# Kernel optimization log

Hardware: AMD Instinct MI355X
Metric: run time of the kernel (lower is better)

## Reference

```python
import jax, jax.numpy as jnp
import numpy as np

D = 256  # in_channels == out_channels -> output_proj is Identity


def setup_inputs() -> dict:
    key = jax.random.key(0)
    ks = jax.random.split(key, 7)
    B, N = 4, 4096
    s = 1.0 / np.sqrt(D)
    return {
        "x": jax.random.normal(ks[0], (B, N, D), dtype=jnp.float32),
        "Wk": jax.random.normal(ks[1], (D, D), dtype=jnp.float32) * s,
        "bk": jax.random.normal(ks[2], (D,), dtype=jnp.float32) * 0.01,
        "Wq": jax.random.normal(ks[3], (D, D), dtype=jnp.float32) * s,
        "bq": jax.random.normal(ks[4], (D,), dtype=jnp.float32) * 0.01,
        "Wv": jax.random.normal(ks[5], (D, D), dtype=jnp.float32) * s,
        "bv": jax.random.normal(ks[6], (D,), dtype=jnp.float32) * 0.01,
    }


def reference(x, Wk, bk, Wq, bq, Wv, bv):
    # Linear projections: torch Linear(x) = x @ W.T + b; here W is stored as [in, out]
    keys = jnp.einsum("bnd,de->bne", x, Wk) + bk
    queries = jnp.einsum("bnd,de->bne", x, Wq) + bq
    values = jnp.einsum("bnd,de->bne", x, Wv) + bv
    scale = 1.0 / jnp.sqrt(jnp.float32(D))
    scores = jnp.einsum("bqd,bkd->bqk", queries, keys) * scale  # [B, N, N]
    attn = jax.nn.softmax(scores, axis=-1)
    out = jnp.einsum("bqk,bkd->bqd", attn, values)
    return out
```

## Files before the change

kernel.cpp:

```cpp
#include <hip/hip_runtime.h>
#include <hip/hip_bf16.h>


typedef __attribute__((ext_vector_type(8))) short bf16x8;
typedef __attribute__((ext_vector_type(4))) float f32x4;

__device__ __forceinline__ float b2f(ushort u){
  union { uint i; float f; } v; v.i = ((uint)u) << 16; return v.f;
}
__device__ __forceinline__ ushort f2b(float f){
  union { float f; uint i; } v; v.f = f;
  uint i = v.i;
  return (ushort)((i + 0x7FFFu + ((i >> 16) & 1u)) >> 16);
}
__device__ __forceinline__ uint pack2(float a, float b){
  return (uint)f2b(a) | ((uint)f2b(b) << 16);
}
__device__ __forceinline__ uint fbits(float f){
  union { float f; uint i; } v; v.f = f; return v.i;
}

__device__ __forceinline__ void gl_lds16(const ushort* g, ushort* l){
  __builtin_amdgcn_global_load_lds(
      (const __attribute__((address_space(1))) uint*)g,
      (__attribute__((address_space(3))) uint*)l, 16, 0, 0);
}

#define Q_SCALE 0.0901684400555602f
#define FIXED_M 16.0f

__global__ __launch_bounds__(256) void transpose_w_kernel(
    const float* __restrict__ Wk, const float* __restrict__ Wq,
    const float* __restrict__ Wv, ushort* __restrict__ Wt){
  __shared__ ushort t[64][72];
  const float* src = (blockIdx.y == 0) ? Wk : (blockIdx.y == 1) ? Wq : Wv;
  ushort* dst = Wt + blockIdx.y * 65536;
  int tile = blockIdx.x;
  int tr = tile >> 2, tc = tile & 3;
  int tid = threadIdx.x;
  for (int i = tid; i < 1024; i += 256){
    int r = i >> 4, ch = i & 15;
    float4 f = *(const float4*)(src + (tr*64 + r)*256 + tc*64 + ch*4);
    uint2 u; u.x = pack2(f.x, f.y); u.y = pack2(f.z, f.w);
    *(uint2*)&t[r][ch*4] = u;
  }
  __syncthreads();
  for (int i = tid; i < 2048; i += 256){
    int c = i >> 5, r2 = (i & 31)*2;
    uint v = (uint)t[r2][c] | ((uint)t[r2+1][c] << 16);
    *(uint*)(dst + (tc*64 + c)*256 + tr*64 + r2) = v;
  }
}

__global__ __launch_bounds__(256) void proj_kernel(
    const float* __restrict__ x, const ushort* __restrict__ Wt,
    const float* __restrict__ bK, const float* __restrict__ bQ,
    const float* __restrict__ bV,
    ushort* __restrict__ Ko, ushort* __restrict__ Qo, ushort* __restrict__ Vt){
  __shared__ ushort xs[64][264];
  __shared__ ushort wt[2][16][264];
  int my = blockIdx.y;
  int n0 = blockIdx.x * 64;
  const ushort* wsrc = Wt + my*65536;
  const float* bias  = (my==0) ? bK : (my==1) ? bQ : bV;

  int tid = threadIdx.x;
  int lane = tid & 63, w = tid >> 6, quad = lane >> 4, l16 = lane & 15;

  for (int i = tid; i < 4096; i += 256){
    int r = i >> 6, ch = i & 63;
    float4 f = *(const float4*)(x + (size_t)(n0 + r)*256 + ch*4);
    uint2 u; u.x = pack2(f.x, f.y); u.y = pack2(f.z, f.w);
    *(uint2*)&xs[r][ch*4] = u;
  }

  int seg0 = tid*2,     r0 = seg0 >> 5, c0 = seg0 & 31;
  int seg1 = tid*2 + 1, r1 = seg1 >> 5, c1 = seg1 & 31;
  {
    uint4 a = *(const uint4*)(wsrc + r0*256 + c0*8);
    uint4 b = *(const uint4*)(wsrc + r1*256 + c1*8);
    *(uint4*)&wt[0][r0][c0*8] = a;
    *(uint4*)&wt[0][r1][c1*8] = b;
  }
  __syncthreads();

  bf16x8 afr[8];
  #pragma unroll
  for (int ks = 0; ks < 8; ks++)
    afr[ks] = *(const bf16x8*)&xs[w*16 + l16][ks*32 + quad*8];

  for (int nt = 0; nt < 16; nt++){
    int cu = nt & 1;
    uint4 wa, wb;
    if (nt < 15){
      const ushort* wn = wsrc + (nt+1)*4096;
      wa = *(const uint4*)(wn + r0*256 + c0*8);
      wb = *(const uint4*)(wn + r1*256 + c1*8);
    }
    f32x4 acc = {0.f, 0.f, 0.f, 0.f};
    #pragma unroll
    for (int ks = 0; ks < 8; ks++){
      bf16x8 bfr = *(const bf16x8*)&wt[cu][l16][ks*32 + quad*8];
      acc = __builtin_amdgcn_mfma_f32_16x16x32_bf16(afr[ks], bfr, acc, 0, 0, 0);
    }
    int e = nt*16 + l16;
    float bv = bias[e];
    if (my == 2){
      int b  = n0 >> 12;
      int nl = (n0 & 4095) + w*16 + quad*4;
      ushort* vb = Vt + (size_t)b*1048576 + (size_t)e*4096 + nl;
      #pragma unroll
      for (int r = 0; r < 4; r++) vb[r] = f2b(acc[r] + bv);
    } else {
      float scale = (my==1) ? Q_SCALE : 1.0f;
      ushort* out = (my==0) ? Ko : Qo;
      #pragma unroll
      for (int r = 0; r < 4; r++){
        int row = n0 + w*16 + quad*4 + r;
        out[(size_t)row*256 + e] = f2b((acc[r] + bv) * scale);
      }
    }
    if (nt < 15){
      *(uint4*)&wt[cu^1][r0][c0*8] = wa;
      *(uint4*)&wt[cu^1][r1][c1*8] = wb;
    }
    __syncthreads();
  }
}

__global__ __launch_bounds__(256, 2) void attn_kernel(
    const ushort* __restrict__ Q, const ushort* __restrict__ K,
    const ushort* __restrict__ Vt,
    float* __restrict__ O0, ushort* __restrict__ Obf, float* __restrict__ lp){
  __shared__ ushort Kbuf[2][8192];
  __shared__ ushort Vbuf[2][8192];
  __shared__ ushort Ps[128][40];

  int bx   = blockIdx.x;
  int bh   = bx & 15;
  int b    = bh >> 2;
  int half = bh & 3;
  int qt   = bx >> 4;
  int tid = threadIdx.x, lane = tid & 63, w = tid >> 6;
  int quad = lane >> 4, l16 = lane & 15;

  const ushort* Qb = Q  + (size_t)(b*4096 + qt*128)*256;
  const ushort* Kb = K  + (size_t)b*4096*256;
  const ushort* Vb = Vt + (size_t)b*256*4096;

  int kOff[4], vOff[4];
  #pragma unroll
  for (int i = 0; i < 4; i++){
    int off16 = (w*4 + i)*64 + lane;
    int krow = off16 >> 5, ks_ = off16 & 31;
    int g    = ks_ ^ (krow & 7);
    kOff[i]  = krow*256 + g*8;
    int sr = off16 >> 3, sl = off16 & 7;
    int xv = sl ^ (sr & 7);
    int d  = sr*2 + ((xv >> 2) & 1), c = xv & 3;
    vOff[i] = d*4096 + c*8;
  }
  int m7 = l16 & 7;
  int kslot[8];
  #pragma unroll
  for (int ks = 0; ks < 8; ks++) kslot[ks] = ((ks*4 + quad) ^ m7) * 8;
  int vlane = (((l16 >> 1)*8) + (((l16 & 1)*4 + quad) ^ (l16 >> 1))) * 8;

  bf16x8 qf[2][8];
  #pragma unroll
  for (int s = 0; s < 2; s++)
    #pragma unroll
    for (int ks = 0; ks < 8; ks++)
      qf[s][ks] = *(const bf16x8*)(Qb + (size_t)(w*32 + s*16 + l16)*256 + ks*32 + quad*8);

  f32x4 of[2][16];
  #pragma unroll
  for (int s = 0; s < 2; s++)
    #pragma unroll
    for (int dt = 0; dt < 16; dt++) of[s][dt] = (f32x4){0.f, 0.f, 0.f, 0.f};
  float l_i[2][4];
  #pragma unroll
  for (int s = 0; s < 2; s++)
    #pragma unroll
    for (int r = 0; r < 4; r++) l_i[s][r] = 0.f;

  int kt0 = half * 32, kt1 = kt0 + 32;

  #pragma unroll
  for (int i = 0; i < 4; i++){
    gl_lds16(Kb + (size_t)kt0*8192 + kOff[i], &Kbuf[0][(w*4 + i)*512]);
    gl_lds16(Vb + (size_t)kt0*32   + vOff[i], &Vbuf[0][(w*4 + i)*512]);
  }
  __syncthreads();

  int cur = 0;
  for (int kt = kt0; kt < kt1; kt++){
    int nxt = cur ^ 1;
    if (kt + 1 < kt1){
      #pragma unroll
      for (int i = 0; i < 4; i++){
        gl_lds16(Kb + (size_t)(kt+1)*8192 + kOff[i], &Kbuf[nxt][(w*4 + i)*512]);
        gl_lds16(Vb + (size_t)(kt+1)*32   + vOff[i], &Vbuf[nxt][(w*4 + i)*512]);
      }
    }
    const ushort* Kc = &Kbuf[cur][0];
    const ushort* Vc = &Vbuf[cur][0];

    f32x4 sf[2][2];
    #pragma unroll
    for (int s = 0; s < 2; s++)
      #pragma unroll
      for (int nt = 0; nt < 2; nt++) sf[s][nt] = (f32x4){0.f, 0.f, 0.f, 0.f};
    #pragma unroll
    for (int nt = 0; nt < 2; nt++){
      const ushort* Kr = Kc + nt*4096 + l16*256;
      #pragma unroll
      for (int ks = 0; ks < 8; ks++){
        bf16x8 bfr = *(const bf16x8*)(Kr + kslot[ks]);
        sf[0][nt] = __builtin_amdgcn_mfma_f32_16x16x32_bf16(qf[0][ks], bfr, sf[0][nt], 0,0,0);
        sf[1][nt] = __builtin_amdgcn_mfma_f32_16x16x32_bf16(qf[1][ks], bfr, sf[1][nt], 0,0,0);
      }
    }

    #pragma unroll
    for (int s = 0; s < 2; s++){
      #pragma unroll
      for (int r = 0; r < 4; r++){
        float p0 = exp2f(sf[s][0][r] - FIXED_M);
        float p1 = exp2f(sf[s][1][r] - FIXED_M);
        l_i[s][r] += p0 + p1;
        uint pb = __builtin_amdgcn_perm(fbits(p1) + 0x8000u,
                                        fbits(p0) + 0x8000u, 0x07060302u);
        ushort* prow = &Ps[w*32 + s*16 + quad*4 + r][0];
        prow[l16]      = (ushort)pb;
        prow[16 + l16] = (ushort)(pb >> 16);
      }
    }

    bf16x8 pf0 = *(const bf16x8*)&Ps[w*32 +      l16][quad*8];
    bf16x8 pf1 = *(const bf16x8*)&Ps[w*32 + 16 + l16][quad*8];
    #pragma unroll
    for (int dt = 0; dt < 16; dt++){
      bf16x8 vf = *(const bf16x8*)(Vc + dt*512 + vlane);
      of[0][dt] = __builtin_amdgcn_mfma_f32_16x16x32_bf16(pf0, vf, of[0][dt], 0, 0, 0);
      of[1][dt] = __builtin_amdgcn_mfma_f32_16x16x32_bf16(pf1, vf, of[1][dt], 0, 0, 0);
    }

    __syncthreads();
    cur = nxt;
  }

  #pragma unroll
  for (int s = 0; s < 2; s++)
    #pragma unroll
    for (int r = 0; r < 4; r++){
      float rs = l_i[s][r];
      #pragma unroll
      for (int msk = 1; msk < 16; msk <<= 1) rs += __shfl_xor(rs, msk, 16);
      l_i[s][r] = rs;
    }

  #pragma unroll
  for (int s = 0; s < 2; s++){
    int gq0 = b*4096 + qt*128 + w*32 + s*16 + quad*4;
    if (l16 == 0){
      #pragma unroll
      for (int r = 0; r < 4; r++)
        lp[(size_t)half*16384 + gq0 + r] = l_i[s][r];
    }
    if (half == 0){
      #pragma unroll
      for (int dt = 0; dt < 16; dt++)
        #pragma unroll
        for (int r = 0; r < 4; r++)
          O0[(size_t)(gq0 + r)*256 + dt*16 + l16] = of[s][dt][r];
    } else {
      ushort* Oh = Obf + (size_t)(half - 1)*16384*256;
      #pragma unroll
      for (int dt = 0; dt < 16; dt++)
        #pragma unroll
        for (int r = 0; r < 4; r++)
          Oh[(size_t)(gq0 + r)*256 + dt*16 + l16] = f2b(of[s][dt][r]);
    }
  }
}

__global__ __launch_bounds__(256) void merge_kernel(
    float* __restrict__ O0, const ushort* __restrict__ Obf,
    const float* __restrict__ lp){
  int t   = blockIdx.x*256 + threadIdx.x;
  int row = t >> 6;
  int c   = (t & 63) * 4;
  float den = lp[row] + lp[16384 + row] + lp[2*16384 + row] + lp[3*16384 + row];
  float rden = 1.0f / den;
  size_t idx = (size_t)row*256 + c;
  float4 acc = *(float4*)&O0[idx];
  #pragma unroll
  for (int h = 1; h < 4; h++){
    ushort4 oh = *(const ushort4*)&Obf[(size_t)(h-1)*16384*256 + idx];
    acc.x += b2f(oh.x); acc.y += b2f(oh.y);
    acc.z += b2f(oh.z); acc.w += b2f(oh.w);
  }
  acc.x *= rden; acc.y *= rden; acc.z *= rden; acc.w *= rden;
  *(float4*)&O0[idx] = acc;
}

extern "C" void kernel_launch(void* const* d_in, const int* in_sizes, int n_in,
                              void* d_out, int out_size, void* d_ws, size_t ws_size,
                              hipStream_t stream){
  const float* x  = (const float*)d_in[0];
  const float* Wk = (const float*)d_in[1];
  const float* bk = (const float*)d_in[2];
  const float* Wq = (const float*)d_in[3];
  const float* bq = (const float*)d_in[4];
  const float* Wv = (const float*)d_in[5];
  const float* bv = (const float*)d_in[6];

  char* ws = (char*)d_ws;
  ushort* Wt  = (ushort*)(ws);
  ushort* Qb  = (ushort*)(ws + (size_t)1*(1u<<20));
  ushort* Kb  = (ushort*)(ws + (size_t)10*(1u<<20));
  ushort* Vtb = (ushort*)(ws + (size_t)19*(1u<<20));
  ushort* Obf = (ushort*)(ws + (size_t)28*(1u<<20));
  float*  lp  = (float*)(ws + (size_t)54*(1u<<20));

  hipLaunchKernelGGL(transpose_w_kernel, dim3(16, 3), dim3(256), 0, stream,
                     Wk, Wq, Wv, Wt);
  hipLaunchKernelGGL(proj_kernel, dim3(256, 3), dim3(256), 0, stream,
                     x, Wt, bk, bq, bv, Kb, Qb, Vtb);
  hipLaunchKernelGGL(attn_kernel, dim3(512), dim3(256), 0, stream,
                     Qb, Kb, Vtb, (float*)d_out, Obf, lp);
  hipLaunchKernelGGL(merge_kernel, dim3(4096), dim3(256), 0, stream,
                     (float*)d_out, Obf, lp);
}
```

Measured before the change: 203.5 us.

## Split attention work across eight waves per block with one 16-row Q slice each

The attention kernel moves from 256 to 512 threads per block. Each wave now owns a single 16-row query slice instead of two, which halves per-wave accumulator and Q-fragment registers and raises the number of resident waves to hide latency. It also wraps the MFMA phases in s_setprio raises. The cost is that each K/V fragment read from LDS now feeds only one MFMA instead of two, so LDS read traffic per FLOP doubles, and more waves take part in each barrier.

After: 285.1 us. 40.1% more time.

```diff
diff --git a/kernel.cpp b/kernel.cpp
--- a/kernel.cpp
+++ b/kernel.cpp
@@ -128,7 +128,7 @@
   }
 }
 
-__global__ __launch_bounds__(256, 2) void attn_kernel(
+__global__ __launch_bounds__(512, 4) void attn_kernel(
     const ushort* __restrict__ Q, const ushort* __restrict__ K,
     const ushort* __restrict__ Vt,
     float* __restrict__ O0, ushort* __restrict__ Obf, float* __restrict__ lp){
@@ -148,10 +148,10 @@
   const ushort* Kb = K  + (size_t)b*4096*256;
   const ushort* Vb = Vt + (size_t)b*256*4096;
 
-  int kOff[4], vOff[4];
-  #pragma unroll
-  for (int i = 0; i < 4; i++){
-    int off16 = (w*4 + i)*64 + lane;
+  int kOff[2], vOff[2];
+  #pragma unroll
+  for (int i = 0; i < 2; i++){
+    int off16 = (w*2 + i)*64 + lane;
     int krow = off16 >> 5, ks_ = off16 & 31;
     int g    = ks_ ^ (krow & 7);
     kOff[i]  = krow*256 + g*8;
@@ -161,35 +161,26 @@
     vOff[i] = d*4096 + c*8;
   }
   int m7 = l16 & 7;
-  int kslot[8];
-  #pragma unroll
-  for (int ks = 0; ks < 8; ks++) kslot[ks] = ((ks*4 + quad) ^ m7) * 8;
   int vlane = (((l16 >> 1)*8) + (((l16 & 1)*4 + quad) ^ (l16 >> 1))) * 8;
 
-  bf16x8 qf[2][8];
-  #pragma unroll
-  for (int s = 0; s < 2; s++)
-    #pragma unroll
-    for (int ks = 0; ks < 8; ks++)
-      qf[s][ks] = *(const bf16x8*)(Qb + (size_t)(w*32 + s*16 + l16)*256 + ks*32 + quad*8);
-
-  f32x4 of[2][16];
-  #pragma unroll
-  for (int s = 0; s < 2; s++)
-    #pragma unroll
-    for (int dt = 0; dt < 16; dt++) of[s][dt] = (f32x4){0.f, 0.f, 0.f, 0.f};
-  float l_i[2][4];
-  #pragma unroll
-  for (int s = 0; s < 2; s++)
-    #pragma unroll
-    for (int r = 0; r < 4; r++) l_i[s][r] = 0.f;
+  bf16x8 qf[8];
+  #pragma unroll
+  for (int ks = 0; ks < 8; ks++)
+    qf[ks] = *(const bf16x8*)(Qb + (size_t)(w*16 + l16)*256 + ks*32 + quad*8);
+
+  f32x4 of[16];
+  #pragma unroll
+  for (int dt = 0; dt < 16; dt++) of[dt] = (f32x4){0.f, 0.f, 0.f, 0.f};
+  float l_i[4];
+  #pragma unroll
+  for (int r = 0; r < 4; r++) l_i[r] = 0.f;
 
   int kt0 = half * 32, kt1 = kt0 + 32;
 
   #pragma unroll
-  for (int i = 0; i < 4; i++){
-    gl_lds16(Kb + (size_t)kt0*8192 + kOff[i], &Kbuf[0][(w*4 + i)*512]);
-    gl_lds16(Vb + (size_t)kt0*32   + vOff[i], &Vbuf[0][(w*4 + i)*512]);
+  for (int i = 0; i < 2; i++){
+    gl_lds16(Kb + (size_t)kt0*8192 + kOff[i], &Kbuf[0][(w*2 + i)*512]);
+    gl_lds16(Vb + (size_t)kt0*32   + vOff[i], &Vbuf[0][(w*2 + i)*512]);
   }
   __syncthreads();
 
@@ -198,89 +189,82 @@
     int nxt = cur ^ 1;
     if (kt + 1 < kt1){
       #pragma unroll
-      for (int i = 0; i < 4; i++){
-        gl_lds16(Kb + (size_t)(kt+1)*8192 + kOff[i], &Kbuf[nxt][(w*4 + i)*512]);
-        gl_lds16(Vb + (size_t)(kt+1)*32   + vOff[i], &Vbuf[nxt][(w*4 + i)*512]);
+      for (int i = 0; i < 2; i++){
+        gl_lds16(Kb + (size_t)(kt+1)*8192 + kOff[i], &Kbuf[nxt][(w*2 + i)*512]);
+        gl_lds16(Vb + (size_t)(kt+1)*32   + vOff[i], &Vbuf[nxt][(w*2 + i)*512]);
       }
     }
     const ushort* Kc = &Kbuf[cur][0];
     const ushort* Vc = &Vbuf[cur][0];
 
-    f32x4 sf[2][2];
-    #pragma unroll
-    for (int s = 0; s < 2; s++)
-      #pragma unroll
-      for (int nt = 0; nt < 2; nt++) sf[s][nt] = (f32x4){0.f, 0.f, 0.f, 0.f};
+    f32x4 sf[2];
+    sf[0] = (f32x4){0.f, 0.f, 0.f, 0.f};
+    sf[1] = (f32x4){0.f, 0.f, 0.f, 0.f};
+    __builtin_amdgcn_s_setprio(1);
     #pragma unroll
     for (int nt = 0; nt < 2; nt++){
       const ushort* Kr = Kc + nt*4096 + l16*256;
       #pragma unroll
       for (int ks = 0; ks < 8; ks++){
-        bf16x8 bfr = *(const bf16x8*)(Kr + kslot[ks]);
-        sf[0][nt] = __builtin_amdgcn_mfma_f32_16x16x32_bf16(qf[0][ks], bfr, sf[0][nt], 0,0,0);
-        sf[1][nt] = __builtin_amdgcn_mfma_f32_16x16x32_bf16(qf[1][ks], bfr, sf[1][nt], 0,0,0);
+        bf16x8 bfr = *(const bf16x8*)(Kr + (((ks*4 + quad) ^ m7) << 3));
+        sf[nt] = __builtin_amdgcn_mfma_f32_16x16x32_bf16(qf[ks], bfr, sf[nt], 0,0,0);
       }
     }
-
-    #pragma unroll
-    for (int s = 0; s < 2; s++){
-      #pragma unroll
-      for (int r = 0; r < 4; r++){
-        float p0 = exp2f(sf[s][0][r] - FIXED_M);
-        float p1 = exp2f(sf[s][1][r] - FIXED_M);
-        l_i[s][r] += p0 + p1;
-        uint pb = __builtin_amdgcn_perm(fbits(p1) + 0x8000u,
-                                        fbits(p0) + 0x8000u, 0x07060302u);
-        ushort* prow = &Ps[w*32 + s*16 + quad*4 + r][0];
-        prow[l16]      = (ushort)pb;
-        prow[16 + l16] = (ushort)(pb >> 16);
-      }
-    }
-
-    bf16x8 pf0 = *(const bf16x8*)&Ps[w*32 +      l16][quad*8];
-    bf16x8 pf1 = *(const bf16x8*)&Ps[w*32 + 16 + l16][quad*8];
+    __builtin_amdgcn_s_setprio(0);
+
+    #pragma unroll
+    for (int r = 0; r < 4; r++){
+      float p0 = exp2f(sf[0][r] - FIXED_M);
+      float p1 = exp2f(sf[1][r] - FIXED_M);
+      l_i[r] += p0 + p1;
+      uint pb = __builtin_amdgcn_perm(fbits(p1) + 0x8000u,
+                                      fbits(p0) + 0x8000u, 0x07060302u);
+      ushort* prow = &Ps[w*16 + quad*4 + r][0];
+      prow[l16]      = (ushort)pb;
+      prow[16 + l16] = (ushort)(pb >> 16);
+    }
+
+    bf16x8 pf = *(const bf16x8*)&Ps[w*16 + l16][quad*8];
+    __builtin_amdgcn_s_setprio(1);
     #pragma unroll
     for (int dt = 0; dt < 16; dt++){
       bf16x8 vf = *(const bf16x8*)(Vc + dt*512 + vlane);
-      of[0][dt] = __builtin_amdgcn_mfma_f32_16x16x32_bf16(pf0, vf, of[0][dt], 0, 0, 0);
-      of[1][dt] = __builtin_amdgcn_mfma_f32_16x16x32_bf16(pf1, vf, of[1][dt], 0, 0, 0);
-    }
+      of[dt] = __builtin_amdgcn_mfma_f32_16x16x32_bf16(pf, vf, of[dt], 0, 0, 0);
+    }
+    __builtin_amdgcn_s_setprio(0);
 
     __syncthreads();
     cur = nxt;
   }
 
   #pragma unroll
-  for (int s = 0; s < 2; s++)
-    #pragma unroll
-    for (int r = 0; r < 4; r++){
-      float rs = l_i[s][r];
-      #pragma unroll
-      for (int msk = 1; msk < 16; msk <<= 1) rs += __shfl_xor(rs, msk, 16);
-      l_i[s][r] = rs;
-    }
-
-  #pragma unroll
-  for (int s = 0; s < 2; s++){
-    int gq0 = b*4096 + qt*128 + w*32 + s*16 + quad*4;
+  for (int r = 0; r < 4; r++){
+    float rs = l_i[r];
+    #pragma unroll
+    for (int msk = 1; msk < 16; msk <<= 1) rs += __shfl_xor(rs, msk, 16);
+    l_i[r] = rs;
+  }
+
+  {
+    int gq0 = b*4096 + qt*128 + w*16 + quad*4;
     if (l16 == 0){
       #pragma unroll
       for (int r = 0; r < 4; r++)
-        lp[(size_t)half*16384 + gq0 + r] = l_i[s][r];
+        lp[(size_t)half*16384 + gq0 + r] = l_i[r];
     }
     if (half == 0){
       #pragma unroll
       for (int dt = 0; dt < 16; dt++)
         #pragma unroll
         for (int r = 0; r < 4; r++)
-          O0[(size_t)(gq0 + r)*256 + dt*16 + l16] = of[s][dt][r];
+          O0[(size_t)(gq0 + r)*256 + dt*16 + l16] = of[dt][r];
     } else {
       ushort* Oh = Obf + (size_t)(half - 1)*16384*256;
       #pragma unroll
       for (int dt = 0; dt < 16; dt++)
         #pragma unroll
         for (int r = 0; r < 4; r++)
-          Oh[(size_t)(gq0 + r)*256 + dt*16 + l16] = f2b(of[s][dt][r]);
+          Oh[(size_t)(gq0 + r)*256 + dt*16 + l16] = f2b(of[dt][r]);
     }
   }
 }
@@ -328,7 +312,7 @@
                      Wk, Wq, Wv, Wt);
   hipLaunchKernelGGL(proj_kernel, dim3(256, 3), dim3(256), 0, stream,
                      x, Wt, bk, bq, bv, Kb, Qb, Vtb);
-  hipLaunchKernelGGL(attn_kernel, dim3(512), dim3(256), 0, stream,
+  hipLaunchKernelGGL(attn_kernel, dim3(512), dim3(512), 0, stream,
                      Qb, Kb, Vtb, (float*)d_out, Obf, lp);
   hipLaunchKernelGGL(merge_kernel, dim3(4096), dim3(256), 0, stream,
                      (float*)d_out, Obf, lp);
```

## Interleave K rows for packed P stores, unroll double-buffer loop, add setprio

Applied to the files above, without the earlier changes.

Reorders the K tile load so LDS row j holds key 2j for the first 16 rows and key 2j+1 for the rest. The two score tiles for a lane then cover adjacent keys, so each P pair goes out as one 32-bit LDS store instead of two 16-bit stores. The key-tile loop is unrolled by two, which makes the buffer index a compile-time constant. MFMA sections are wrapped in s_setprio to favour matrix issue across waves. This trades a more intricate index mapping for fewer LDS store instructions and cheaper address arithmetic.

New measurement: 302.0 us. +48.4%, slower.

```diff
diff --git a/kernel.cpp b/kernel.cpp
--- a/kernel.cpp
+++ b/kernel.cpp
@@ -153,8 +153,9 @@
   for (int i = 0; i < 4; i++){
     int off16 = (w*4 + i)*64 + lane;
     int krow = off16 >> 5, ks_ = off16 & 31;
+    int key  = (krow < 16) ? (krow*2) : ((krow - 16)*2 + 1);
     int g    = ks_ ^ (krow & 7);
-    kOff[i]  = krow*256 + g*8;
+    kOff[i]  = key*256 + g*8;
     int sr = off16 >> 3, sl = off16 & 7;
     int xv = sl ^ (sr & 7);
     int d  = sr*2 + ((xv >> 2) & 1), c = xv & 3;
@@ -193,61 +194,63 @@
   }
   __syncthreads();
 
-  int cur = 0;
-  for (int kt = kt0; kt < kt1; kt++){
-    int nxt = cur ^ 1;
-    if (kt + 1 < kt1){
-      #pragma unroll
-      for (int i = 0; i < 4; i++){
-        gl_lds16(Kb + (size_t)(kt+1)*8192 + kOff[i], &Kbuf[nxt][(w*4 + i)*512]);
-        gl_lds16(Vb + (size_t)(kt+1)*32   + vOff[i], &Vbuf[nxt][(w*4 + i)*512]);
-      }
-    }
-    const ushort* Kc = &Kbuf[cur][0];
-    const ushort* Vc = &Vbuf[cur][0];
-
-    f32x4 sf[2][2];
-    #pragma unroll
-    for (int s = 0; s < 2; s++)
-      #pragma unroll
-      for (int nt = 0; nt < 2; nt++) sf[s][nt] = (f32x4){0.f, 0.f, 0.f, 0.f};
-    #pragma unroll
-    for (int nt = 0; nt < 2; nt++){
-      const ushort* Kr = Kc + nt*4096 + l16*256;
-      #pragma unroll
-      for (int ks = 0; ks < 8; ks++){
-        bf16x8 bfr = *(const bf16x8*)(Kr + kslot[ks]);
-        sf[0][nt] = __builtin_amdgcn_mfma_f32_16x16x32_bf16(qf[0][ks], bfr, sf[0][nt], 0,0,0);
-        sf[1][nt] = __builtin_amdgcn_mfma_f32_16x16x32_bf16(qf[1][ks], bfr, sf[1][nt], 0,0,0);
-      }
-    }
-
-    #pragma unroll
-    for (int s = 0; s < 2; s++){
-      #pragma unroll
-      for (int r = 0; r < 4; r++){
-        float p0 = exp2f(sf[s][0][r] - FIXED_M);
-        float p1 = exp2f(sf[s][1][r] - FIXED_M);
-        l_i[s][r] += p0 + p1;
-        uint pb = __builtin_amdgcn_perm(fbits(p1) + 0x8000u,
-                                        fbits(p0) + 0x8000u, 0x07060302u);
-        ushort* prow = &Ps[w*32 + s*16 + quad*4 + r][0];
-        prow[l16]      = (ushort)pb;
-        prow[16 + l16] = (ushort)(pb >> 16);
-      }
-    }
-
-    bf16x8 pf0 = *(const bf16x8*)&Ps[w*32 +      l16][quad*8];
-    bf16x8 pf1 = *(const bf16x8*)&Ps[w*32 + 16 + l16][quad*8];
-    #pragma unroll
-    for (int dt = 0; dt < 16; dt++){
-      bf16x8 vf = *(const bf16x8*)(Vc + dt*512 + vlane);
-      of[0][dt] = __builtin_amdgcn_mfma_f32_16x16x32_bf16(pf0, vf, of[0][dt], 0, 0, 0);
-      of[1][dt] = __builtin_amdgcn_mfma_f32_16x16x32_bf16(pf1, vf, of[1][dt], 0, 0, 0);
-    }
-
-    __syncthreads();
-    cur = nxt;
+  for (int ktp = kt0; ktp < kt1; ktp += 2){
+    #pragma unroll
+    for (int kk = 0; kk < 2; kk++){
+      const int C  = kk;
+      int kt = ktp + kk;
+      if (kt + 1 < kt1){
+        #pragma unroll
+        for (int i = 0; i < 4; i++){
+          gl_lds16(Kb + (size_t)(kt+1)*8192 + kOff[i], &Kbuf[C^1][(w*4 + i)*512]);
+          gl_lds16(Vb + (size_t)(kt+1)*32   + vOff[i], &Vbuf[C^1][(w*4 + i)*512]);
+        }
+      }
+
+      f32x4 sf[2][2];
+      #pragma unroll
+      for (int s = 0; s < 2; s++)
+        #pragma unroll
+        for (int nt = 0; nt < 2; nt++) sf[s][nt] = (f32x4){0.f, 0.f, 0.f, 0.f};
+      __builtin_amdgcn_s_setprio(1);
+      #pragma unroll
+      for (int nt = 0; nt < 2; nt++){
+        const ushort* Kr = &Kbuf[C][nt*4096 + l16*256];
+        #pragma unroll
+        for (int ks = 0; ks < 8; ks++){
+          bf16x8 bfr = *(const bf16x8*)(Kr + kslot[ks]);
+          sf[0][nt] = __builtin_amdgcn_mfma_f32_16x16x32_bf16(qf[0][ks], bfr, sf[0][nt], 0,0,0);
+          sf[1][nt] = __builtin_amdgcn_mfma_f32_16x16x32_bf16(qf[1][ks], bfr, sf[1][nt], 0,0,0);
+        }
+      }
+      __builtin_amdgcn_s_setprio(0);
+
+      #pragma unroll
+      for (int s = 0; s < 2; s++){
+        #pragma unroll
+        for (int r = 0; r < 4; r++){
+          float p0 = exp2f(sf[s][0][r] - FIXED_M);
+          float p1 = exp2f(sf[s][1][r] - FIXED_M);
+          l_i[s][r] += p0 + p1;
+          uint pb = __builtin_amdgcn_perm(fbits(p1) + 0x8000u,
+                                          fbits(p0) + 0x8000u, 0x07060302u);
+          *(uint*)&Ps[w*32 + s*16 + quad*4 + r][2*l16] = pb;
+        }
+      }
+
+      bf16x8 pf0 = *(const bf16x8*)&Ps[w*32 +      l16][quad*8];
+      bf16x8 pf1 = *(const bf16x8*)&Ps[w*32 + 16 + l16][quad*8];
+      __builtin_amdgcn_s_setprio(1);
+      #pragma unroll
+      for (int dt = 0; dt < 16; dt++){
+        bf16x8 vf = *(const bf16x8*)(&Vbuf[C][0] + dt*512 + vlane);
+        of[0][dt] = __builtin_amdgcn_mfma_f32_16x16x32_bf16(pf0, vf, of[0][dt], 0, 0, 0);
+        of[1][dt] = __builtin_amdgcn_mfma_f32_16x16x32_bf16(pf1, vf, of[1][dt], 0, 0, 0);
+      }
+      __builtin_amdgcn_s_setprio(0);
+
+      __syncthreads();
+    }
   }
 
   #pragma unroll
```
